# Kernel optimization log

Hardware: AMD Instinct MI355X
Metric: run time of the kernel (lower is better)

The kernel has to match this reference:

```python
import jax, jax.numpy as jnp
import numpy as np

# NF4 codebook (bitsandbytes nf4 data type, 16 levels)
NF4_TABLE = np.array([
    -1.0, -0.6961928009986877, -0.5250730514526367, -0.39491748809814453,
    -0.28444138169288635, -0.18477343022823334, -0.09105003625154495, 0.0,
    0.07958029955625534, 0.16093020141124725, 0.24611230194568634,
    0.33791524171829224, 0.44070982933044434, 0.5626170039176941,
    0.7229568362236023, 1.0], dtype=np.float32)

BLOCKSIZE = 64
SCALING = 32.0 / 16.0  # lora_alpha / r


def setup_inputs() -> dict:
    key = jax.random.key(0)
    k1, k2, k3, k4, k5 = jax.random.split(key, 5)
    tokens, in_f, out_f, r = 256, 4096, 11008, 16
    x = jax.random.normal(k1, (tokens, in_f), dtype=jnp.float32)
    q_codes = jax.random.randint(k2, (out_f, in_f), 0, 16, dtype=jnp.int32)
    absmax = jax.random.uniform(k3, (out_f, in_f // BLOCKSIZE), dtype=jnp.float32)
    lora_A = jax.random.normal(k4, (r, in_f), dtype=jnp.float32) * (1.0 / np.sqrt(in_f))
    lora_B = jax.random.normal(k5, (out_f, r), dtype=jnp.float32) * 0.02
    return {"x": x, "q_codes": q_codes, "absmax": absmax,
            "lora_A": lora_A, "lora_B": lora_B}


def reference(x, q_codes, absmax, lora_A, lora_B):
    out_f, in_f = q_codes.shape
    nf4 = jnp.asarray(NF4_TABLE, dtype=x.dtype)
    # Dequantize: codebook lookup, then per-block absmax scale.
    W = nf4[q_codes].reshape(out_f, in_f // BLOCKSIZE, BLOCKSIZE)
    W = (W * absmax[:, :, None]).reshape(out_f, in_f)  # [out_f, in_f]
    # Base 4-bit linear (no bias in bnb Linear4bit default here).
    base = x @ W.T  # [tokens, out_f]
    # LoRA path: dropout p=0 is identity in eval; scaling = alpha/r.
    lora = (x @ lora_A.T) @ lora_B.T  # [tokens, r] -> [tokens, out_f]
    return base + lora * jnp.asarray(SCALING, dtype=x.dtype)
```

## Files before the change

kernel.cpp:

```cpp
#include <hip/hip_runtime.h>
#include <hip/hip_fp16.h>

typedef unsigned int uint;
typedef unsigned short ushort;

typedef __attribute__((ext_vector_type(8))) _Float16 f16x8;
typedef __attribute__((ext_vector_type(4))) float f32x4;

#define TOK 256
#define OUTF 11008
#define INF 4096
#define BM 256
#define BN 64
#define NT2 172

__device__ __constant__ float NF4_TBL[16] = {
    -1.0f, -0.6961928009986877f, -0.5250730514526367f, -0.39491748809814453f,
    -0.28444138169288635f, -0.18477343022823334f, -0.09105003625154495f, 0.0f,
    0.07958029955625534f, 0.16093020141124725f, 0.24611230194568634f,
    0.33791524171829224f, 0.44070982933044434f, 0.5626170039176941f,
    0.7229568362236023f, 1.0f};

__device__ __forceinline__ ushort f2h(float f) {
  return __half_as_ushort(__float2half(f));
}

__device__ __forceinline__ void async_cp16(const void* g, void* l) {
  __builtin_amdgcn_global_load_lds(
      (const __attribute__((address_space(1))) uint*)g,
      (__attribute__((address_space(3))) uint*)l, 16, 0, 0);
}

__device__ __forceinline__ float nf4v(int c, int tbits) {
  return __int_as_float(__builtin_amdgcn_ds_bpermute(c << 2, tbits));
}

__device__ __forceinline__ uint2 dq4(int4 c, __half2 ax2, int tbits) {
  __half2 h0 = __floats2half2_rn(nf4v(c.x, tbits), nf4v(c.y, tbits));
  __half2 h1 = __floats2half2_rn(nf4v(c.z, tbits), nf4v(c.w, tbits));
  h0 = __hmul2(h0, ax2);
  h1 = __hmul2(h1, ax2);
  union { __half2 h[2]; uint2 u; } r;
  r.h[0] = h0; r.h[1] = h1;
  return r.u;
}

__global__ void prep_kernel(const float4* __restrict__ x4, ushort4* __restrict__ xh4,
                            const float4* __restrict__ lB4, ushort4* __restrict__ lBh4) {
  const int stride = gridDim.x * blockDim.x;
  const int t0 = blockIdx.x * blockDim.x + threadIdx.x;
  for (int i = t0; i < TOK * INF / 4; i += stride) {
    float4 v = x4[i];
    ushort4 o;
    o.x = f2h(v.x); o.y = f2h(v.y); o.z = f2h(v.z); o.w = f2h(v.w);
    xh4[i] = o;
  }
  for (int i = t0; i < OUTF * 16; i += stride) {
    int n = i >> 4, jq = i & 15;
    ushort4 o = {0, 0, 0, 0};
    if (jq < 4) {
      float4 v = lB4[n * 4 + jq];
      o.x = f2h(v.x); o.y = f2h(v.y); o.z = f2h(v.z); o.w = f2h(v.w);
    }
    lBh4[i] = o;
  }
}

__global__ __launch_bounds__(1024)
void xa_kernel(const float* __restrict__ x, const float* __restrict__ lA,
               ushort* __restrict__ xa2) {
  const int m = blockIdx.x;
  const int t = threadIdx.x;
  const float4* x4 = (const float4*)(x + (size_t)m * INF);
  const float4* lA4 = (const float4*)lA;
  float4 xv = x4[t];
  float acc[16];
#pragma unroll
  for (int j = 0; j < 16; ++j) {
    float4 a = lA4[j * (INF / 4) + t];
    acc[j] = xv.x * a.x + xv.y * a.y + xv.z * a.z + xv.w * a.w;
  }
#pragma unroll
  for (int j = 0; j < 16; ++j)
#pragma unroll
    for (int s = 32; s > 0; s >>= 1) acc[j] += __shfl_xor(acc[j], s, 64);
  __shared__ float red[16][16];
  const int w = t >> 6, l = t & 63;
  if (l == 0) {
#pragma unroll
    for (int j = 0; j < 16; ++j) red[w][j] = acc[j];
  }
  __syncthreads();
  if (t < 64) {
    ushort v = 0;
    if (t < 16) {
      float s = 0.f;
#pragma unroll
      for (int w2 = 0; w2 < 16; ++w2) s += red[w2][t];
      v = f2h(2.0f * s);
    }
    xa2[m * 64 + t] = v;
  }
}

__global__ __launch_bounds__(256, 3)
void gemm_kernel(const int* __restrict__ qc, const float* __restrict__ am,
                 const ushort* __restrict__ xh, const ushort* __restrict__ lBh,
                 const ushort* __restrict__ xa2, float* __restrict__ dest, int nst) {
  __shared__ ushort Abuf[BM * 64];
  __shared__ ushort Bbuf[64 * 64];
  __shared__ float Qax[1024];

  const int tid = threadIdx.x;
  const int w = tid >> 6;
  const int l = tid & 63;
  const int chunk = l >> 4;
  const int rlo = l & 15;
  const int split = blockIdx.x / NT2;
  const int ntile = blockIdx.x - split * NT2;
  const int n0 = ntile * BN;
  const int kb0 = split * nst;

  const int tbits = __float_as_int(NF4_TBL[l & 15]);

  const int arow = w * 8 + (l >> 3);
  const int acol = ((l & 7) ^ (l >> 3)) << 3;
  int aoff[2][4];
#pragma unroll
  for (int ks2 = 0; ks2 < 2; ++ks2) {
    const int cc = ks2 * 4 + chunk;
#pragma unroll
    for (int mt = 0; mt < 4; ++mt)
      aoff[ks2][mt] = (w * 64 + mt * 16 + rlo) * 64 + ((cc ^ (l & 7)) << 3);
  }

  const int qrg = tid >> 4;
  const int qch = tid & 15;
  const int* qbase[4];
  int bdst[4];
#pragma unroll
  for (int p = 0; p < 4; ++p) {
    int r = p * 16 + qrg;
    qbase[p] = qc + (size_t)(n0 + r) * INF + kb0 * 64 + qch * 4;
    bdst[p] = r * 64 + (((qch >> 1) ^ (r & 7)) << 3) + (qch & 1) * 4;
  }

  int boff[2][4];
#pragma unroll
  for (int ks2 = 0; ks2 < 2; ++ks2)
#pragma unroll
    for (int nt = 0; nt < 4; ++nt)
      boff[ks2][nt] = (nt * 16 + rlo) * 64 + (((ks2 * 4 + chunk) ^ (rlo & 7)) << 3);

  f32x4 acc[4][4];
#pragma unroll
  for (int mt = 0; mt < 4; ++mt)
#pragma unroll
    for (int nt = 0; nt < 4; ++nt) acc[mt][nt] = (f32x4){0.f, 0.f, 0.f, 0.f};

  if (w == 0) {
#pragma unroll
    for (int j = 0; j < 4; ++j)
      async_cp16(am + (size_t)(n0 + l) * 64 + kb0 + j * 4, (char*)Qax + j * 1024);
  }
#pragma unroll
  for (int i = 0; i < 8; ++i) {
    const ushort* g = xh + (size_t)(i * 32 + arow) * INF + kb0 * 64 + acol;
    async_cp16(g, &Abuf[(i * 256 + w * 64) * 8]);
  }
  int4 qreg[4];
#pragma unroll
  for (int p = 0; p < 4; ++p) qreg[p] = *(const int4*)(qbase[p]);

  for (int s = 0; s < nst; ++s) {
    __syncthreads();

    const int sl = s & 15;
#pragma unroll
    for (int p = 0; p < 4; ++p) {
      int r = p * 16 + qrg;
      __half2 ax2 = __float2half2_rn(Qax[(sl >> 2) * 256 + r * 4 + (sl & 3)]);
      *(uint2*)&Bbuf[bdst[p]] = dq4(qreg[p], ax2, tbits);
    }
    f16x8 areg[2][4];
#pragma unroll
    for (int ks2 = 0; ks2 < 2; ++ks2)
#pragma unroll
      for (int mt = 0; mt < 4; ++mt) areg[ks2][mt] = *(const f16x8*)&Abuf[aoff[ks2][mt]];

    __syncthreads();

    if (s + 1 < nst) {
      const int kb = kb0 + s + 1;
#pragma unroll
      for (int i = 0; i < 8; ++i) {
        const ushort* g = xh + (size_t)(i * 32 + arow) * INF + kb * 64 + acol;
        async_cp16(g, &Abuf[(i * 256 + w * 64) * 8]);
      }
#pragma unroll
      for (int p = 0; p < 4; ++p) qreg[p] = *(const int4*)(qbase[p] + (s + 1) * 64);
      if (((s + 1) & 15) == 0 && w == 0) {
#pragma unroll
        for (int j = 0; j < 4; ++j)
          async_cp16(am + (size_t)(n0 + l) * 64 + kb0 + s + 1 + j * 4, (char*)Qax + j * 1024);
      }
    }

#pragma unroll
    for (int ks2 = 0; ks2 < 2; ++ks2) {
      f16x8 b[4];
#pragma unroll
      for (int nt = 0; nt < 4; ++nt) b[nt] = *(const f16x8*)&Bbuf[boff[ks2][nt]];
#pragma unroll
      for (int mt = 0; mt < 4; ++mt)
#pragma unroll
        for (int nt = 0; nt < 4; ++nt)
          acc[mt][nt] = __builtin_amdgcn_mfma_f32_16x16x32_f16(areg[ks2][mt], b[nt], acc[mt][nt], 0, 0, 0);
    }
  }

  if (split == 0) {
    f16x8 a_l[4], b_l[4];
#pragma unroll
    for (int mt = 0; mt < 4; ++mt)
      a_l[mt] = *(const f16x8*)(xa2 + (size_t)(w * 64 + mt * 16 + rlo) * 64 + chunk * 8);
#pragma unroll
    for (int nt = 0; nt < 4; ++nt)
      b_l[nt] = *(const f16x8*)(lBh + (size_t)(n0 + nt * 16 + rlo) * 64 + chunk * 8);
#pragma unroll
    for (int mt = 0; mt < 4; ++mt)
#pragma unroll
      for (int nt = 0; nt < 4; ++nt)
        acc[mt][nt] = __builtin_amdgcn_mfma_f32_16x16x32_f16(a_l[mt], b_l[nt], acc[mt][nt], 0, 0, 0);
  }

  float* dst = dest + (size_t)split * TOK * OUTF;
#pragma unroll
  for (int mt = 0; mt < 4; ++mt) {
#pragma unroll
    for (int nt = 0; nt < 4; ++nt) {
      int c = n0 + nt * 16 + rlo;
#pragma unroll
      for (int r = 0; r < 4; ++r) {
        int row = w * 64 + mt * 16 + chunk * 4 + r;
        dst[(size_t)row * OUTF + c] = acc[mt][nt][r];
      }
    }
  }
}

__global__ void reduce_kernel(const float4* __restrict__ part, float4* __restrict__ out,
                              int ks) {
  const int QN = TOK * OUTF / 4;
  int i = blockIdx.x * blockDim.x + threadIdx.x;
  if (i < QN) {
    float4 s = part[i];
    for (int s2 = 1; s2 < ks; ++s2) {
      float4 p = part[(size_t)s2 * QN + i];
      s.x += p.x; s.y += p.y; s.z += p.z; s.w += p.w;
    }
    out[i] = s;
  }
}

extern "C" void kernel_launch(void* const* d_in, const int* in_sizes, int n_in,
                              void* d_out, int out_size, void* d_ws, size_t ws_size,
                              hipStream_t stream) {
  const float* x = (const float*)d_in[0];
  const int* qc = (const int*)d_in[1];
  const float* am = (const float*)d_in[2];
  const float* lA = (const float*)d_in[3];
  const float* lB = (const float*)d_in[4];
  float* out = (float*)d_out;

  const size_t off_lB = (size_t)TOK * INF * 2;
  const size_t off_xa2 = off_lB + (size_t)OUTF * 64 * 2;
  const size_t off_part = off_xa2 + (size_t)TOK * 64 * 2;
  const size_t part_bytes = (size_t)TOK * OUTF * 4;

  ushort* xh = (ushort*)d_ws;
  ushort* lBh = (ushort*)((char*)d_ws + off_lB);
  ushort* xa2 = (ushort*)((char*)d_ws + off_xa2);
  float* part = (float*)((char*)d_ws + off_part);

  int ks = 1;
  if (ws_size >= off_part + 4 * part_bytes) ks = 4;
  else if (ws_size >= off_part + 2 * part_bytes) ks = 2;
  float* dest = (ks == 1) ? out : part;

  prep_kernel<<<2048, 256, 0, stream>>>((const float4*)x, (ushort4*)xh,
                                        (const float4*)lB, (ushort4*)lBh);
  xa_kernel<<<TOK, 1024, 0, stream>>>(x, lA, xa2);
  gemm_kernel<<<NT2 * ks, 256, 0, stream>>>(qc, am, xh, lBh, xa2, dest, 64 / ks);
  if (ks > 1)
    reduce_kernel<<<(TOK * OUTF / 4 + 255) / 256, 256, 0, stream>>>((const float4*)part,
                                                                    (float4*)out, ks);
}
```

Baseline: 312.3 us.

## Pack int32 NF4 codes into 4-bit nibbles in prep kernel before GEMM

Adds a pass in the prep kernel that packs eight int32 NF4 codes into one 32-bit word and stores the packed weights in workspace. The GEMM now loads one uint2 per thread per step, eight codes per word, instead of four int4 loads, and writes wider LDS stores. The aim is to cut GEMM global load volume and instruction count. The full int32 codes are still read once per call in prep, and the packed copy is written and read back, so total traffic rises slightly.

```diff
diff --git a/kernel.cpp b/kernel.cpp
--- a/kernel.cpp
+++ b/kernel.cpp
@@ -35,20 +35,20 @@
   return __int_as_float(__builtin_amdgcn_ds_bpermute(c << 2, tbits));
 }
 
-__device__ __forceinline__ uint2 dq4(int4 c, __half2 ax2, int tbits) {
-  __half2 h0 = __floats2half2_rn(nf4v(c.x, tbits), nf4v(c.y, tbits));
-  __half2 h1 = __floats2half2_rn(nf4v(c.z, tbits), nf4v(c.w, tbits));
-  h0 = __hmul2(h0, ax2);
-  h1 = __hmul2(h1, ax2);
-  union { __half2 h[2]; uint2 u; } r;
-  r.h[0] = h0; r.h[1] = h1;
-  return r.u;
-}
-
 __global__ void prep_kernel(const float4* __restrict__ x4, ushort4* __restrict__ xh4,
-                            const float4* __restrict__ lB4, ushort4* __restrict__ lBh4) {
+                            const float4* __restrict__ lB4, ushort4* __restrict__ lBh4,
+                            const int4* __restrict__ qc4, uint* __restrict__ q4) {
   const int stride = gridDim.x * blockDim.x;
   const int t0 = blockIdx.x * blockDim.x + threadIdx.x;
+  for (int i = t0; i < OUTF * (INF / 8); i += stride) {
+    int4 a = qc4[(size_t)i * 2];
+    int4 b = qc4[(size_t)i * 2 + 1];
+    uint p = (uint)(a.x & 15) | ((uint)(a.y & 15) << 4) | ((uint)(a.z & 15) << 8) |
+             ((uint)(a.w & 15) << 12) | ((uint)(b.x & 15) << 16) |
+             ((uint)(b.y & 15) << 20) | ((uint)(b.z & 15) << 24) |
+             ((uint)(b.w & 15) << 28);
+    q4[i] = p;
+  }
   for (int i = t0; i < TOK * INF / 4; i += stride) {
     float4 v = x4[i];
     ushort4 o;
@@ -104,7 +104,7 @@
 }
 
 __global__ __launch_bounds__(256, 3)
-void gemm_kernel(const int* __restrict__ qc, const float* __restrict__ am,
+void gemm_kernel(const uint* __restrict__ q4, const float* __restrict__ am,
                  const ushort* __restrict__ xh, const ushort* __restrict__ lBh,
                  const ushort* __restrict__ xa2, float* __restrict__ dest, int nst) {
   __shared__ ushort Abuf[BM * 64];
@@ -134,16 +134,11 @@
       aoff[ks2][mt] = (w * 64 + mt * 16 + rlo) * 64 + ((cc ^ (l & 7)) << 3);
   }
 
-  const int qrg = tid >> 4;
-  const int qch = tid & 15;
-  const int* qbase[4];
-  int bdst[4];
-#pragma unroll
-  for (int p = 0; p < 4; ++p) {
-    int r = p * 16 + qrg;
-    qbase[p] = qc + (size_t)(n0 + r) * INF + kb0 * 64 + qch * 4;
-    bdst[p] = r * 64 + (((qch >> 1) ^ (r & 7)) << 3) + (qch & 1) * 4;
-  }
+  const int qr = tid >> 2;
+  const int oc2 = (tid & 3) << 1;
+  const uint* qb = q4 + (size_t)(n0 + qr) * (INF / 8) + (size_t)kb0 * 8 + oc2;
+  const int bd0 = qr * 64 + ((oc2 ^ (qr & 7)) << 3);
+  const int bd1 = qr * 64 + (((oc2 + 1) ^ (qr & 7)) << 3);
 
   int boff[2][4];
 #pragma unroll
@@ -168,19 +163,26 @@
     const ushort* g = xh + (size_t)(i * 32 + arow) * INF + kb0 * 64 + acol;
     async_cp16(g, &Abuf[(i * 256 + w * 64) * 8]);
   }
-  int4 qreg[4];
-#pragma unroll
-  for (int p = 0; p < 4; ++p) qreg[p] = *(const int4*)(qbase[p]);
+  uint2 qreg = *(const uint2*)qb;
 
   for (int s = 0; s < nst; ++s) {
     __syncthreads();
 
     const int sl = s & 15;
-#pragma unroll
-    for (int p = 0; p < 4; ++p) {
-      int r = p * 16 + qrg;
-      __half2 ax2 = __float2half2_rn(Qax[(sl >> 2) * 256 + r * 4 + (sl & 3)]);
-      *(uint2*)&Bbuf[bdst[p]] = dq4(qreg[p], ax2, tbits);
+    const __half2 ax2 = __float2half2_rn(Qax[(sl >> 2) * 256 + qr * 4 + (sl & 3)]);
+    {
+      const uint q0 = qreg.x, q1 = qreg.y;
+      union { __half2 h[4]; uint4 u; } r0, r1;
+      r0.h[0] = __hmul2(__floats2half2_rn(nf4v(q0 & 15, tbits), nf4v((q0 >> 4) & 15, tbits)), ax2);
+      r0.h[1] = __hmul2(__floats2half2_rn(nf4v((q0 >> 8) & 15, tbits), nf4v((q0 >> 12) & 15, tbits)), ax2);
+      r0.h[2] = __hmul2(__floats2half2_rn(nf4v((q0 >> 16) & 15, tbits), nf4v((q0 >> 20) & 15, tbits)), ax2);
+      r0.h[3] = __hmul2(__floats2half2_rn(nf4v((q0 >> 24) & 15, tbits), nf4v(q0 >> 28, tbits)), ax2);
+      r1.h[0] = __hmul2(__floats2half2_rn(nf4v(q1 & 15, tbits), nf4v((q1 >> 4) & 15, tbits)), ax2);
+      r1.h[1] = __hmul2(__floats2half2_rn(nf4v((q1 >> 8) & 15, tbits), nf4v((q1 >> 12) & 15, tbits)), ax2);
+      r1.h[2] = __hmul2(__floats2half2_rn(nf4v((q1 >> 16) & 15, tbits), nf4v((q1 >> 20) & 15, tbits)), ax2);
+      r1.h[3] = __hmul2(__floats2half2_rn(nf4v((q1 >> 24) & 15, tbits), nf4v(q1 >> 28, tbits)), ax2);
+      *(uint4*)&Bbuf[bd0] = r0.u;
+      *(uint4*)&Bbuf[bd1] = r1.u;
     }
     f16x8 areg[2][4];
 #pragma unroll
@@ -197,8 +199,7 @@
         const ushort* g = xh + (size_t)(i * 32 + arow) * INF + kb * 64 + acol;
         async_cp16(g, &Abuf[(i * 256 + w * 64) * 8]);
       }
-#pragma unroll
-      for (int p = 0; p < 4; ++p) qreg[p] = *(const int4*)(qbase[p] + (s + 1) * 64);
+      qreg = *(const uint2*)(qb + (s + 1) * 8);
       if (((s + 1) & 15) == 0 && w == 0) {
 #pragma unroll
         for (int j = 0; j < 4; ++j)
@@ -275,12 +276,14 @@
 
   const size_t off_lB = (size_t)TOK * INF * 2;
   const size_t off_xa2 = off_lB + (size_t)OUTF * 64 * 2;
-  const size_t off_part = off_xa2 + (size_t)TOK * 64 * 2;
+  const size_t off_q4 = off_xa2 + (size_t)TOK * 64 * 2;
+  const size_t off_part = off_q4 + (size_t)OUTF * (INF / 8) * 4;
   const size_t part_bytes = (size_t)TOK * OUTF * 4;
 
   ushort* xh = (ushort*)d_ws;
   ushort* lBh = (ushort*)((char*)d_ws + off_lB);
   ushort* xa2 = (ushort*)((char*)d_ws + off_xa2);
+  uint* q4 = (uint*)((char*)d_ws + off_q4);
   float* part = (float*)((char*)d_ws + off_part);
 
   int ks = 1;
@@ -289,9 +292,10 @@
   float* dest = (ks == 1) ? out : part;
 
   prep_kernel<<<2048, 256, 0, stream>>>((const float4*)x, (ushort4*)xh,
-                                        (const float4*)lB, (ushort4*)lBh);
+                                        (const float4*)lB, (ushort4*)lBh,
+                                        (const int4*)qc, q4);
   xa_kernel<<<TOK, 1024, 0, stream>>>(x, lA, xa2);
-  gemm_kernel<<<NT2 * ks, 256, 0, stream>>>(qc, am, xh, lBh, xa2, dest, 64 / ks);
+  gemm_kernel<<<NT2 * ks, 256, 0, stream>>>(q4, am, xh, lBh, xa2, dest, 64 / ks);
   if (ks > 1)
     reduce_kernel<<<(TOK * OUTF / 4 + 255) / 256, 256, 0, stream>>>((const float4*)part,
                                                                     (float4*)out, ks);
```

Result: slower. 323.8 us (+3.7%).
